# Kernel optimization log

Measured on AMD Instinct MI355X. Metric: run time of the kernel, lower is better.

Reference implementation:

```python
import jax, jax.numpy as jnp
import numpy as np

B, T, DIM = 8, 4096, 1024
HEADS = 16
WS = [10, 20]
SHIFTS = [5, 10]
DIM_IN = DIM // 2        # bottleneck_ratio=0.5
DIM_BR = DIM_IN // 2     # per-branch channels
H_BR = HEADS // 2        # per-branch heads
EPS = 1e-6


def setup_inputs() -> dict:
    key = jax.random.key(0)
    ks = jax.random.split(key, 12)
    w = lambda k, s: (jax.random.normal(k, s) * 0.02).astype(jnp.float32)
    z = lambda n: jnp.zeros((n,), jnp.float32)
    return {
        "x": jax.random.normal(ks[0], (B, T, DIM), jnp.float32),
        "down_w": w(ks[1], (DIM, DIM_IN)), "down_b": z(DIM_IN),
        "up_w": w(ks[2], (DIM_IN, DIM)), "up_b": z(DIM),
        "norm1_w": jnp.ones((DIM_IN,), jnp.float32),
        "norm2_w": jnp.ones((DIM,), jnp.float32),
        "qkv1_w": w(ks[3], (DIM_BR, 3 * DIM_BR)), "qkv1_b": z(3 * DIM_BR),
        "proj1_w": w(ks[4], (DIM_BR, DIM_BR)), "proj1_b": z(DIM_BR),
        "rpb1": w(ks[5], (2 * WS[0] - 1, H_BR)),
        "qkv2_w": w(ks[6], (DIM_BR, 3 * DIM_BR)), "qkv2_b": z(3 * DIM_BR),
        "proj2_w": w(ks[7], (DIM_BR, DIM_BR)), "proj2_b": z(DIM_BR),
        "rpb2": w(ks[8], (2 * WS[1] - 1, H_BR)),
        "ffn_w1": w(ks[9], (DIM, 2 * DIM)), "ffn_b1": z(2 * DIM),
        "ffn_w2": w(ks[10], (2 * DIM, DIM)), "ffn_b2": z(DIM),
    }


def rmsnorm(x, w):
    return x * jax.lax.rsqrt(jnp.mean(x * x, axis=-1, keepdims=True) + EPS) * w


def _branch(x, window, shift, qkv_w, qkv_b, pw, pb, rpb, heads):
    # x: [B, T, C]; shifted-window attention along T with relative position bias
    Bx, Tn, C = x.shape
    pad = (-Tn) % window
    xp = jnp.pad(x, ((0, 0), (0, pad), (0, 0)))
    Tp = Tn + pad
    nW = Tp // window
    hd = C // heads
    scale = hd ** -0.5

    if shift > 0:
        xp = jnp.roll(xp, -shift, axis=1)
        m = np.zeros(Tp, np.float32)
        m[Tp - window:Tp - shift] = 1.0
        m[Tp - shift:] = 2.0
        mw = m.reshape(nW, window)
        amask = jnp.asarray(np.where(mw[:, :, None] != mw[:, None, :], -100.0, 0.0).astype(np.float32))  # [nW,w,w]
    else:
        amask = None

    xw = xp.reshape(Bx, nW, window, C)
    qkv = (xw @ qkv_w + qkv_b).reshape(Bx, nW, window, 3, heads, hd)
    q, k, v = qkv[:, :, :, 0], qkv[:, :, :, 1], qkv[:, :, :, 2]  # [B,nW,w,h,hd]

    attn = jnp.einsum('bnqhd,bnkhd->bnhqk', q * scale, k)  # [B,nW,h,w,w]

    coords = np.arange(window)
    ridx = coords[:, None] - coords[None, :] + window - 1      # [w,w]
    bias = jnp.transpose(rpb[ridx], (2, 0, 1))                 # [h,w,w]
    attn = attn + bias[None, None]
    if amask is not None:
        attn = attn + amask[None, :, None]

    attn = jax.nn.softmax(attn, axis=-1)
    out = jnp.einsum('bnhqk,bnkhd->bnqhd', attn, v).reshape(Bx, nW, window, C)
    out = out @ pw + pb
    out = out.reshape(Bx, Tp, C)
    if shift > 0:
        out = jnp.roll(out, shift, axis=1)
    return out[:, :Tn]


def reference(x, down_w, down_b, up_w, up_b, norm1_w, norm2_w,
              qkv1_w, qkv1_b, proj1_w, proj1_b, rpb1,
              qkv2_w, qkv2_b, proj2_w, proj2_b, rpb2,
              ffn_w1, ffn_b1, ffn_w2, ffn_b2):
    residual = x
    xi = rmsnorm(x @ down_w + down_b, norm1_w)           # [B,T,DIM_IN]
    x1, x2 = xi[..., :DIM_BR], xi[..., DIM_BR:]
    o1 = _branch(x1, WS[0], SHIFTS[0], qkv1_w, qkv1_b, proj1_w, proj1_b, rpb1, H_BR)
    o2 = _branch(x2, WS[1], SHIFTS[1], qkv2_w, qkv2_b, proj2_w, proj2_b, rpb2, H_BR)
    xc = jnp.concatenate([o1, o2], axis=-1) @ up_w + up_b
    x = residual + xc
    h = rmsnorm(x, norm2_w)
    ffn = jax.nn.gelu(h @ ffn_w1 + ffn_b1, approximate=False) @ ffn_w2 + ffn_b2
    return x + ffn
```

## Files before the change

kernel.cpp:

```cpp
#include <hip/hip_runtime.h>
#include <hip/hip_bf16.h>
#include <math.h>

typedef __bf16 bf16x8_t __attribute__((ext_vector_type(8)));
typedef float f32x4_t __attribute__((ext_vector_type(4)));
typedef __hip_bfloat16 bf16;

__device__ __forceinline__ void gload_lds16(const bf16* gsrc, unsigned short* ldst) {
  __builtin_amdgcn_global_load_lds(
      (const __attribute__((address_space(1))) unsigned int*)gsrc,
      (__attribute__((address_space(3))) unsigned int*)ldst, 16, 0, 0);
}

__global__ __launch_bounds__(256) void f2b_kernel(const float* __restrict__ in,
                                                  bf16* __restrict__ out, size_t n) {
  size_t i = ((size_t)blockIdx.x * 256 + threadIdx.x) * 4;
  if (i + 4 <= n) {
    float4 v = *reinterpret_cast<const float4*>(in + i);
    union { bf16 b[4]; ushort4 u; } cv;
    cv.b[0] = __float2bfloat16(v.x);
    cv.b[1] = __float2bfloat16(v.y);
    cv.b[2] = __float2bfloat16(v.z);
    cv.b[3] = __float2bfloat16(v.w);
    *reinterpret_cast<ushort4*>(out + i) = cv.u;
  } else {
    for (; i < n; ++i) out[i] = __float2bfloat16(in[i]);
  }
}

__global__ __launch_bounds__(256) void transpose_f2b_kernel(const float* __restrict__ in,
                                                            bf16* __restrict__ out,
                                                            int K, int N) {
  __shared__ float t[32][33];
  int n0 = blockIdx.x * 32, k0 = blockIdx.y * 32;
  int tx = threadIdx.x & 31, ty = threadIdx.x >> 5;
#pragma unroll
  for (int i = 0; i < 32; i += 8)
    t[ty + i][tx] = in[(size_t)(k0 + ty + i) * N + n0 + tx];
  __syncthreads();
#pragma unroll
  for (int i = 0; i < 32; i += 8)
    out[(size_t)(n0 + ty + i) * K + k0 + tx] = __float2bfloat16(t[tx][ty + i]);
}

__global__ __launch_bounds__(256) void rmsnorm_kernel(const float* __restrict__ in,
                                                      const float* __restrict__ w,
                                                      bf16* __restrict__ out, int C) {
  int row = blockIdx.x;
  const float* r = in + (size_t)row * C;
  int tid = threadIdx.x;
  float ss = 0.f;
  for (int c = tid; c < C; c += 256) { float v = r[c]; ss += v * v; }
#pragma unroll
  for (int o = 32; o > 0; o >>= 1) ss += __shfl_down(ss, o, 64);
  __shared__ float part[4];
  if ((tid & 63) == 0) part[tid >> 6] = ss;
  __syncthreads();
  float inv = rsqrtf((part[0] + part[1] + part[2] + part[3]) / (float)C + 1e-6f);
  bf16* orow = out + (size_t)row * C;
  for (int c = tid; c < C; c += 256) orow[c] = __float2bfloat16(r[c] * inv * w[c]);
}

__global__ __launch_bounds__(256) void gather_kernel(const bf16* __restrict__ xi,
                                                     bf16* __restrict__ xb,
                                                     int Tp, int Tn, int shift, int coff) {
  size_t i = (size_t)blockIdx.x * 256 + threadIdx.x;
  int c = (int)(i & 255);
  size_t bt = i >> 8;
  int t = (int)(bt % (size_t)Tp);
  int b = (int)(bt / (size_t)Tp);
  int src = t + shift; if (src >= Tp) src -= Tp;
  bf16 v = __float2bfloat16(0.f);
  if (src < Tn) v = xi[(((size_t)b * Tn + src) << 9) + coff + c];
  xb[i] = v;
}

template <int W, int SHIFT>
__global__ void attn_kernel(const bf16* __restrict__ qkv, const float* __restrict__ rpb,
                            bf16* __restrict__ out, int nW, int Tp) {
  int blk = blockIdx.x;
  int b = blk / nW, n = blk % nW;
  int pair = threadIdx.x;
  if (pair >= 8 * W) return;
  int h = pair / W, qi = pair % W;
  size_t base = ((size_t)b * Tp + (size_t)n * W) * 768;
  float qv[32];
#pragma unroll
  for (int d = 0; d < 32; ++d) qv[d] = __bfloat162float(qkv[base + (size_t)qi * 768 + h * 32 + d]);
  const float scale = 0.17677669529663689f;
  float sc[W];
  float mx = -1e30f;
  for (int k = 0; k < W; ++k) {
    const bf16* kr = qkv + base + (size_t)k * 768 + 256 + h * 32;
    float dot = 0.f;
#pragma unroll
    for (int d = 0; d < 32; ++d) dot += qv[d] * __bfloat162float(kr[d]);
    float s = dot * scale + rpb[(qi - k + W - 1) * 8 + h];
    if (n == nW - 1) {
      bool lq = qi < (W - SHIFT), lk = k < (W - SHIFT);
      if (lq != lk) s -= 100.0f;
    }
    sc[k] = s;
    mx = fmaxf(mx, s);
  }
  float l = 0.f;
  for (int k = 0; k < W; ++k) { sc[k] = expf(sc[k] - mx); l += sc[k]; }
  float inv = 1.0f / l;
  float ov[32];
#pragma unroll
  for (int d = 0; d < 32; ++d) ov[d] = 0.f;
  for (int k = 0; k < W; ++k) {
    const bf16* vr = qkv + base + (size_t)k * 768 + 512 + h * 32;
    float p = sc[k];
#pragma unroll
    for (int d = 0; d < 32; ++d) ov[d] += p * __bfloat162float(vr[d]);
  }
  bf16* orow = out + ((size_t)b * Tp + (size_t)n * W + qi) * 256 + h * 32;
#pragma unroll
  for (int d = 0; d < 32; ++d) orow[d] = __float2bfloat16(ov[d] * inv);
}

template <int MODE>
__global__ __launch_bounds__(256) void gemm_kernel(
    const bf16* __restrict__ A, const bf16* __restrict__ Wt,
    const float* __restrict__ bias,
    float* outF, bf16* outB, const float* resid,
    int M, int N, int K, int ldc, int Tp, int Tn, int shift, int coff) {
  __shared__ unsigned short lA[128 * 32];
  __shared__ unsigned short lB[128 * 32];
  int tid = threadIdx.x;
  int wave = tid >> 6, lane = tid & 63;
  int m0 = blockIdx.y * 128, n0 = blockIdx.x * 128;
  int wm = (wave >> 1) * 64, wn = (wave & 1) * 64;
  int ml = lane & 15, koff = (lane >> 4) * 8;
  f32x4_t acc[4][4] = {};

  int lrow = lane >> 2;
  int lcol = (lane & 3) * 8;
  int ar0 = wave * 32;

  for (int k0 = 0; k0 < K; k0 += 32) {
    __syncthreads();
#pragma unroll
    for (int j = 0; j < 2; ++j) {
      int r = ar0 + j * 16;
      int gr = m0 + r + lrow; if (gr > M - 1) gr = M - 1;
      gload_lds16(A + (size_t)gr * K + k0 + lcol, &lA[r * 32]);
      int nr = n0 + r + lrow;
      gload_lds16(Wt + (size_t)nr * K + k0 + lcol, &lB[r * 32]);
    }
    __syncthreads();

    bf16x8_t fa[4], fb[4];
#pragma unroll
    for (int t = 0; t < 4; ++t) {
      fa[t] = *reinterpret_cast<const bf16x8_t*>(&lA[(wm + t * 16 + ml) * 32 + koff]);
      fb[t] = *reinterpret_cast<const bf16x8_t*>(&lB[(wn + t * 16 + ml) * 32 + koff]);
    }
#pragma unroll
    for (int mt = 0; mt < 4; ++mt)
#pragma unroll
      for (int nt = 0; nt < 4; ++nt)
        acc[mt][nt] = __builtin_amdgcn_mfma_f32_16x16x32_bf16(fa[mt], fb[nt], acc[mt][nt], 0, 0, 0);
  }

  int rbase = (lane >> 4) * 4;
#pragma unroll
  for (int mt = 0; mt < 4; ++mt)
#pragma unroll
    for (int nt = 0; nt < 4; ++nt)
#pragma unroll
      for (int i = 0; i < 4; ++i) {
        int row = m0 + wm + mt * 16 + rbase + i;
        int col = n0 + wn + nt * 16 + ml;
        if (row >= M) continue;
        float v = acc[mt][nt][i] + bias[col];
        if (MODE == 0) {
          outF[(size_t)row * ldc + col] = v;
        } else if (MODE == 1) {
          outB[(size_t)row * ldc + col] = __float2bfloat16(v);
        } else if (MODE == 2) {
          outF[(size_t)row * ldc + col] = v + resid[(size_t)row * ldc + col];
        } else if (MODE == 3) {
          v = 0.5f * v * (1.0f + erff(v * 0.70710678118654752f));
          outB[(size_t)row * ldc + col] = __float2bfloat16(v);
        } else if (MODE == 5) {
          int b = row / Tp;
          int t = row - b * Tp;
          int i2 = t + shift; if (i2 >= Tp) i2 -= Tp;
          if (i2 < Tn)
            outB[((size_t)b * Tn + i2) * ldc + coff + col] = __float2bfloat16(v);
        }
      }
}

extern "C" void kernel_launch(void* const* d_in, const int* in_sizes, int n_in,
                              void* d_out, int out_size, void* d_ws, size_t ws_size,
                              hipStream_t stream) {
  const float* x       = (const float*)d_in[0];
  const float* down_w  = (const float*)d_in[1];
  const float* down_b  = (const float*)d_in[2];
  const float* up_w    = (const float*)d_in[3];
  const float* up_b    = (const float*)d_in[4];
  const float* norm1_w = (const float*)d_in[5];
  const float* norm2_w = (const float*)d_in[6];
  const float* qkv1_w  = (const float*)d_in[7];
  const float* qkv1_b  = (const float*)d_in[8];
  const float* proj1_w = (const float*)d_in[9];
  const float* proj1_b = (const float*)d_in[10];
  const float* rpb1    = (const float*)d_in[11];
  const float* qkv2_w  = (const float*)d_in[12];
  const float* qkv2_b  = (const float*)d_in[13];
  const float* proj2_w = (const float*)d_in[14];
  const float* proj2_b = (const float*)d_in[15];
  const float* rpb2    = (const float*)d_in[16];
  const float* ffn_w1  = (const float*)d_in[17];
  const float* ffn_b1  = (const float*)d_in[18];
  const float* ffn_w2  = (const float*)d_in[19];
  const float* ffn_b2  = (const float*)d_in[20];
  float* out = (float*)d_out;

  const int Bb = 8, T = 4096, DIM = 1024, DIM_IN = 512;
  const int Tp = 4100, Tn = T;
  const int M  = Bb * T;
  const int Mp = Bb * Tp;
  const int nW1 = Tp / 10, nW2 = Tp / 20;

  char* ws = (char*)d_ws;
  const size_t MB = 1ull << 20;
  size_t wo = 0;
  auto walloc = [&](size_t elems) {
    bf16* p = (bf16*)(ws + wo);
    wo += ((elems * 2 + 255) & ~(size_t)255);
    return p;
  };
  bf16* w_down  = walloc(1024 * 512);
  bf16* w_up    = walloc(512 * 1024);
  bf16* w_qkv1  = walloc(256 * 768);
  bf16* w_proj1 = walloc(256 * 256);
  bf16* w_qkv2  = walloc(256 * 768);
  bf16* w_proj2 = walloc(256 * 256);
  bf16* w_ffn1  = walloc(1024 * 2048);
  bf16* w_ffn2  = walloc(2048 * 1024);
  bf16*  xbf     = (bf16*)(ws + 12 * MB);
  bf16*  xb1     = (bf16*)(ws + 12 * MB);
  bf16*  xb2     = (bf16*)(ws + 29 * MB);
  bf16*  att1    = (bf16*)(ws + 46 * MB);
  bf16*  att2    = (bf16*)(ws + 63 * MB);
  float* y1      = (float*)(ws + 80 * MB);
  bf16*  concatb = (bf16*)(ws + 80 * MB);
  bf16*  hbuf    = (bf16*)(ws + 80 * MB);
  bf16*  xi      = (bf16*)(ws + 144 * MB);
  bf16*  qkv1buf = (bf16*)(ws + 176 * MB);
  bf16*  qkv2buf = (bf16*)(ws + 225 * MB);
  bf16*  gbuf    = (bf16*)(ws + 144 * MB);

  auto cvt = [&](const float* src, bf16* dst, size_t n) {
    int grid = (int)((n / 4 + 255) / 256);
    hipLaunchKernelGGL(f2b_kernel, dim3(grid), dim3(256), 0, stream, src, dst, n);
  };
  auto tr = [&](const float* src, bf16* dst, int K, int N) {
    hipLaunchKernelGGL(transpose_f2b_kernel, dim3(N / 32, K / 32), dim3(256), 0, stream,
                       src, dst, K, N);
  };
  cvt(x, xbf, (size_t)M * DIM);
  tr(down_w, w_down, 1024, 512);
  tr(up_w, w_up, 512, 1024);
  tr(qkv1_w, w_qkv1, 256, 768);
  tr(proj1_w, w_proj1, 256, 256);
  tr(qkv2_w, w_qkv2, 256, 768);
  tr(proj2_w, w_proj2, 256, 256);
  tr(ffn_w1, w_ffn1, 1024, 2048);
  tr(ffn_w2, w_ffn2, 2048, 1024);

  auto gemm = [&](auto modeTag, const bf16* A, const bf16* Wt, const float* bias,
                  float* oF, bf16* oB, const float* res,
                  int Mm, int Nn, int Kk, int ldc, int tp, int tn, int sh, int co) {
    constexpr int MODE = decltype(modeTag)::value;
    hipLaunchKernelGGL((gemm_kernel<MODE>), dim3(Nn / 128, (Mm + 127) / 128), dim3(256), 0,
                       stream, A, Wt, bias, oF, oB, res, Mm, Nn, Kk, ldc, tp, tn, sh, co);
  };
  using I0 = std::integral_constant<int, 0>;
  using I1 = std::integral_constant<int, 1>;
  using I2 = std::integral_constant<int, 2>;
  using I3 = std::integral_constant<int, 3>;
  using I5 = std::integral_constant<int, 5>;

  gemm(I0{}, xbf, w_down, down_b, y1, nullptr, nullptr, M, DIM_IN, DIM, DIM_IN, 0, 0, 0, 0);
  hipLaunchKernelGGL(rmsnorm_kernel, dim3(M), dim3(256), 0, stream, y1, norm1_w, xi, DIM_IN);
  hipLaunchKernelGGL(gather_kernel, dim3(Mp), dim3(256), 0, stream, xi, xb1, Tp, Tn, 5, 0);
  hipLaunchKernelGGL(gather_kernel, dim3(Mp), dim3(256), 0, stream, xi, xb2, Tp, Tn, 10, 256);
  gemm(I1{}, xb1, w_qkv1, qkv1_b, nullptr, qkv1buf, nullptr, Mp, 768, 256, 768, 0, 0, 0, 0);
  gemm(I1{}, xb2, w_qkv2, qkv2_b, nullptr, qkv2buf, nullptr, Mp, 768, 256, 768, 0, 0, 0, 0);
  hipLaunchKernelGGL((attn_kernel<10, 5>), dim3(Bb * nW1), dim3(128), 0, stream,
                     qkv1buf, rpb1, att1, nW1, Tp);
  hipLaunchKernelGGL((attn_kernel<20, 10>), dim3(Bb * nW2), dim3(192), 0, stream,
                     qkv2buf, rpb2, att2, nW2, Tp);
  gemm(I5{}, att1, w_proj1, proj1_b, nullptr, concatb, nullptr, Mp, 256, 256, 512, Tp, Tn, 5, 0);
  gemm(I5{}, att2, w_proj2, proj2_b, nullptr, concatb, nullptr, Mp, 256, 256, 512, Tp, Tn, 10, 256);
  gemm(I2{}, concatb, w_up, up_b, out, nullptr, x, M, DIM, DIM_IN, DIM, 0, 0, 0, 0);
  hipLaunchKernelGGL(rmsnorm_kernel, dim3(M), dim3(256), 0, stream, out, norm2_w, hbuf, DIM);
  gemm(I3{}, hbuf, w_ffn1, ffn_b1, nullptr, gbuf, nullptr, M, 2048, DIM, 2048, 0, 0, 0, 0);
  gemm(I2{}, gbuf, w_ffn2, ffn_b2, out, nullptr, out, M, DIM, 2048, DIM, 0, 0, 0, 0);
  (void)in_sizes; (void)n_in; (void)out_size; (void)ws_size;
}
```

Before: 1.544 ms.

## Vectorize attention loads/stores, remap head-major threads, and XCD-swizzle GEMM grid

The attention kernel now loads q/k/v rows as 16-byte vectors and writes output with vector stores. It remaps threads so consecutive lanes cover different heads of the same query, fully unrolls the key loops and uses fast __expf. The GEMM launch is flattened to a 1D grid with an XCD-aware swizzle, so blocks on the same chiplet share row tiles for L2 reuse. Risks are higher register pressure from the unrolled float arrays and slight precision loss from __expf.

```diff
diff --git a/kernel.cpp b/kernel.cpp
--- a/kernel.cpp
+++ b/kernel.cpp
@@ -1,6 +1,7 @@
 #include <hip/hip_runtime.h>
 #include <hip/hip_bf16.h>
 #include <math.h>
+#include <type_traits>
 
 typedef __bf16 bf16x8_t __attribute__((ext_vector_type(8)));
 typedef float f32x4_t __attribute__((ext_vector_type(4)));
@@ -10,6 +11,12 @@
   __builtin_amdgcn_global_load_lds(
       (const __attribute__((address_space(1))) unsigned int*)gsrc,
       (__attribute__((address_space(3))) unsigned int*)ldst, 16, 0, 0);
+}
+
+__device__ __forceinline__ void b2f8(uint4 u, float* f) {
+  const bf16* b = (const bf16*)&u;
+#pragma unroll
+  for (int j = 0; j < 8; ++j) f[j] = __bfloat162float(b[j]);
 }
 
 __global__ __launch_bounds__(256) void f2b_kernel(const float* __restrict__ in,
@@ -82,21 +89,27 @@
   int b = blk / nW, n = blk % nW;
   int pair = threadIdx.x;
   if (pair >= 8 * W) return;
-  int h = pair / W, qi = pair % W;
+  int h = pair & 7, qi = pair >> 3;
   size_t base = ((size_t)b * Tp + (size_t)n * W) * 768;
+  const uint4* qp = reinterpret_cast<const uint4*>(qkv + base + (size_t)qi * 768 + h * 32);
   float qv[32];
 #pragma unroll
-  for (int d = 0; d < 32; ++d) qv[d] = __bfloat162float(qkv[base + (size_t)qi * 768 + h * 32 + d]);
+  for (int j = 0; j < 4; ++j) b2f8(qp[j], qv + j * 8);
   const float scale = 0.17677669529663689f;
   float sc[W];
   float mx = -1e30f;
+  const bool lastw = (n == nW - 1);
+#pragma unroll
   for (int k = 0; k < W; ++k) {
-    const bf16* kr = qkv + base + (size_t)k * 768 + 256 + h * 32;
+    const uint4* kp = reinterpret_cast<const uint4*>(qkv + base + (size_t)k * 768 + 256 + h * 32);
+    float kf[32];
+#pragma unroll
+    for (int j = 0; j < 4; ++j) b2f8(kp[j], kf + j * 8);
     float dot = 0.f;
 #pragma unroll
-    for (int d = 0; d < 32; ++d) dot += qv[d] * __bfloat162float(kr[d]);
+    for (int d = 0; d < 32; ++d) dot += qv[d] * kf[d];
     float s = dot * scale + rpb[(qi - k + W - 1) * 8 + h];
-    if (n == nW - 1) {
+    if (lastw) {
       bool lq = qi < (W - SHIFT), lk = k < (W - SHIFT);
       if (lq != lk) s -= 100.0f;
     }
@@ -104,20 +117,30 @@
     mx = fmaxf(mx, s);
   }
   float l = 0.f;
-  for (int k = 0; k < W; ++k) { sc[k] = expf(sc[k] - mx); l += sc[k]; }
+#pragma unroll
+  for (int k = 0; k < W; ++k) { sc[k] = __expf(sc[k] - mx); l += sc[k]; }
   float inv = 1.0f / l;
   float ov[32];
 #pragma unroll
   for (int d = 0; d < 32; ++d) ov[d] = 0.f;
+#pragma unroll
   for (int k = 0; k < W; ++k) {
-    const bf16* vr = qkv + base + (size_t)k * 768 + 512 + h * 32;
+    const uint4* vp = reinterpret_cast<const uint4*>(qkv + base + (size_t)k * 768 + 512 + h * 32);
+    float vf[32];
+#pragma unroll
+    for (int j = 0; j < 4; ++j) b2f8(vp[j], vf + j * 8);
     float p = sc[k];
 #pragma unroll
-    for (int d = 0; d < 32; ++d) ov[d] += p * __bfloat162float(vr[d]);
+    for (int d = 0; d < 32; ++d) ov[d] += p * vf[d];
   }
   bf16* orow = out + ((size_t)b * Tp + (size_t)n * W + qi) * 256 + h * 32;
 #pragma unroll
-  for (int d = 0; d < 32; ++d) orow[d] = __float2bfloat16(ov[d] * inv);
+  for (int j = 0; j < 4; ++j) {
+    union { bf16 b[8]; uint4 u; } cv;
+#pragma unroll
+    for (int d = 0; d < 8; ++d) cv.b[d] = __float2bfloat16(ov[j * 8 + d] * inv);
+    *reinterpret_cast<uint4*>(orow + j * 8) = cv.u;
+  }
 }
 
 template <int MODE>
@@ -125,12 +148,24 @@
     const bf16* __restrict__ A, const bf16* __restrict__ Wt,
     const float* __restrict__ bias,
     float* outF, bf16* outB, const float* resid,
-    int M, int N, int K, int ldc, int Tp, int Tn, int shift, int coff) {
+    int M, int N, int K, int ldc, int gx, int gy, int swiz,
+    int Tp, int Tn, int shift, int coff) {
   __shared__ unsigned short lA[128 * 32];
   __shared__ unsigned short lB[128 * 32];
+  int f = blockIdx.x;
+  int bx, by;
+  if (swiz) {
+    int xcd = f & 7, s = f >> 3;
+    int rows = gy >> 3;
+    bx = s % gx;
+    by = xcd * rows + s / gx;
+  } else {
+    bx = f % gx;
+    by = f / gx;
+  }
   int tid = threadIdx.x;
   int wave = tid >> 6, lane = tid & 63;
-  int m0 = blockIdx.y * 128, n0 = blockIdx.x * 128;
+  int m0 = by * 128, n0 = bx * 128;
   int wm = (wave >> 1) * 64, wn = (wave & 1) * 64;
   int ml = lane & 15, koff = (lane >> 4) * 8;
   f32x4_t acc[4][4] = {};
@@ -277,8 +312,11 @@
                   float* oF, bf16* oB, const float* res,
                   int Mm, int Nn, int Kk, int ldc, int tp, int tn, int sh, int co) {
     constexpr int MODE = decltype(modeTag)::value;
-    hipLaunchKernelGGL((gemm_kernel<MODE>), dim3(Nn / 128, (Mm + 127) / 128), dim3(256), 0,
-                       stream, A, Wt, bias, oF, oB, res, Mm, Nn, Kk, ldc, tp, tn, sh, co);
+    int gx = Nn / 128, gy = (Mm + 127) / 128;
+    int swiz = (gy % 8 == 0) ? 1 : 0;
+    hipLaunchKernelGGL((gemm_kernel<MODE>), dim3(gx * gy), dim3(256), 0,
+                       stream, A, Wt, bias, oF, oB, res, Mm, Nn, Kk, ldc,
+                       gx, gy, swiz, tp, tn, sh, co);
   };
   using I0 = std::integral_constant<int, 0>;
   using I1 = std::integral_constant<int, 1>;
```

Measured after the change: 1.555 ms. Within noise of the previous version (+0.7%).
